# Optimization experiments

Measured on AMD Instinct MI355X. Metric: run time of the kernel, lower is better.

The kernel has to match this reference:

```python
import jax, jax.numpy as jnp
import numpy as np

N_VARS = 2048
N_LAYERS = 8
NODES = 4096
FAN_IN = 4
BATCH = 8192


def setup_inputs() -> dict:
    key = jax.random.key(0)
    k1, k2 = jax.random.split(key)
    x = jax.random.uniform(k1, (BATCH, N_VARS), dtype=jnp.float32)
    marginalized_variables = jnp.zeros((N_VARS,), dtype=bool)
    # child_idx[l, n, f]: index of the f-th child of node n in layer l,
    # pointing into the previous layer's 4096 outputs (leaves for l=0).
    child_idx = jax.random.randint(k2, (N_LAYERS, NODES, FAN_IN), 0, NODES, dtype=jnp.int64)
    return {"x": x, "marginalized_variables": marginalized_variables, "child_idx": child_idx}


def reference(x, marginalized_variables, child_idx):
    # Leaf literals: positive literal = x[:, v], negative literal = 1 - x[:, v].
    # Marginalized variables output 1.0 for both literals.
    leaves = jnp.concatenate([x, 1.0 - x], axis=1)            # [B, 2V]
    marg = jnp.tile(marginalized_variables, 2)                 # [2V]
    cur = jnp.where(marg[None, :], jnp.ones((), dtype=leaves.dtype), leaves)
    n_layers = child_idx.shape[0]
    for l in range(n_layers):  # fixed small layer loop; each layer fully vectorized
        gathered = cur[:, child_idx[l]]                        # [B, NODES, FAN_IN]
        if l % 2 == 0:  # AND layer: product of children
            cur = jnp.prod(gathered, axis=-1)                  # [B, NODES]
        else:            # OR layer: sum of children
            cur = jnp.sum(gathered, axis=-1)                   # [B, NODES]
    # Root OR node over the final layer -> [B, 1]
    return jnp.sum(cur, axis=1, keepdims=True)
```

## Files before the change

### kernel.cpp

```cpp
#include <hip/hip_runtime.h>

constexpr int N_VARS   = 2048;
constexpr int NODES    = 4096;
constexpr int N_LAYERS = 8;
constexpr int BATCH    = 8192;
constexpr int THREADS  = 256;
constexpr int RPB      = 2;
constexpr int NPT      = NODES / THREADS;

__device__ __forceinline__ float bflo(unsigned w) { return __uint_as_float(w << 16); }
__device__ __forceinline__ float bfhi(unsigned w) { return __uint_as_float(w & 0xffff0000u); }
__device__ __forceinline__ unsigned bfpack(float a, float b) {
  unsigned ua = __float_as_uint(a), ub = __float_as_uint(b);
  ua = (ua + 0x7fffu + ((ua >> 16) & 1u)) >> 16;
  ub = (ub + 0x7fffu + ((ub >> 16) & 1u)) & 0xffff0000u;
  return ua | ub;
}

template <int MODE>
__device__ __forceinline__ ushort4 get_idx(const void* p, int n) {
  if (MODE == 0) return ((const ushort4*)p)[n];
  if (MODE == 1) {
    int4 c = ((const int4*)p)[n];
    return make_ushort4((unsigned short)c.x, (unsigned short)c.y,
                        (unsigned short)c.z, (unsigned short)c.w);
  }
  const int* q = (const int*)p + (size_t)n * 8;
  return make_ushort4((unsigned short)q[0], (unsigned short)q[2],
                      (unsigned short)q[4], (unsigned short)q[6]);
}
template <int MODE> __device__ __forceinline__ size_t layer_bytes() {
  return MODE == 0 ? (size_t)NODES * 8 : MODE == 1 ? (size_t)NODES * 16
                                                   : (size_t)NODES * 32;
}

template <int MODE>
__device__ __forceinline__ void prod_pass(const float2* A, unsigned* B,
                                          const void* idx, int t) {
#pragma unroll
  for (int i = 0; i < NPT; ++i) {
    const int n = t + i * THREADS;
    ushort4 c = get_idx<MODE>(idx, n);
    float2 a = A[c.x], b = A[c.y], d = A[c.z], e = A[c.w];
    B[n] = bfpack(a.x * b.x * d.x * e.x, a.y * b.y * d.y * e.y);
  }
}

template <int MODE>
__device__ __forceinline__ void sum_pass(const unsigned* B, float2* A,
                                         const void* idx, int t) {
#pragma unroll
  for (int i = 0; i < NPT; ++i) {
    const int n = t + i * THREADS;
    ushort4 c = get_idx<MODE>(idx, n);
    unsigned a = B[c.x], b = B[c.y], d = B[c.z], e = B[c.w];
    A[n] = make_float2(bflo(a) + bflo(b) + bflo(d) + bflo(e),
                       bfhi(a) + bfhi(b) + bfhi(d) + bfhi(e));
  }
}

template <int MODE>
__device__ __forceinline__ void spn_body(const float* __restrict__ x,
                                         const unsigned char* __restrict__ marg,
                                         const void* __restrict__ idx,
                                         float* __restrict__ out,
                                         float2* A,
                                         unsigned* B) {
  const int t = threadIdx.x;
  const int row0 = blockIdx.x * RPB;
  const float* x0 = x + (size_t)row0 * N_VARS;
  const float* x1 = x0 + N_VARS;

#pragma unroll
  for (int i = 0; i < N_VARS / THREADS; ++i) {
    const int j = t + i * THREADS;
    const float a = x0[j], b = x1[j];
    const bool m = marg[j] != 0;
    A[j]          = make_float2(m ? 1.f : a,       m ? 1.f : b);
    A[N_VARS + j] = make_float2(m ? 1.f : 1.f - a, m ? 1.f : 1.f - b);
  }

  const char* ib = (const char*)idx;
  const size_t LB = layer_bytes<MODE>();
  __syncthreads();
  prod_pass<MODE>(A, B, ib + 0 * LB, t); __syncthreads();
  sum_pass <MODE>(B, A, ib + 1 * LB, t); __syncthreads();
  prod_pass<MODE>(A, B, ib + 2 * LB, t); __syncthreads();
  sum_pass <MODE>(B, A, ib + 3 * LB, t); __syncthreads();
  prod_pass<MODE>(A, B, ib + 4 * LB, t); __syncthreads();
  sum_pass <MODE>(B, A, ib + 5 * LB, t); __syncthreads();
  prod_pass<MODE>(A, B, ib + 6 * LB, t); __syncthreads();

  float s0 = 0.f, s1 = 0.f;
  {
    const void* L7 = ib + 7 * LB;
#pragma unroll
    for (int i = 0; i < NPT; ++i) {
      const int n = t + i * THREADS;
      ushort4 c = get_idx<MODE>(L7, n);
      unsigned a = B[c.x], b = B[c.y], d = B[c.z], e = B[c.w];
      s0 += bflo(a) + bflo(b) + bflo(d) + bflo(e);
      s1 += bfhi(a) + bfhi(b) + bfhi(d) + bfhi(e);
    }
  }
#pragma unroll
  for (int off = 32; off > 0; off >>= 1) {
    s0 += __shfl_down(s0, off);
    s1 += __shfl_down(s1, off);
  }
  if ((t & 63) == 0) A[t >> 6] = make_float2(s0, s1);
  __syncthreads();
  if (t == 0) {
    float2 tot = A[0];
#pragma unroll
    for (int w = 1; w < THREADS / 64; ++w) { tot.x += A[w].x; tot.y += A[w].y; }
    out[row0]     = tot.x;
    out[row0 + 1] = tot.y;
  }
}

__global__ __launch_bounds__(THREADS) void spn_packed(
    const float* __restrict__ x, const unsigned char* __restrict__ marg,
    const ushort4* __restrict__ idx, float* __restrict__ out) {
  __shared__ float2   A[NODES];
  __shared__ unsigned B[NODES];
  spn_body<0>(x, marg, idx, out, A, B);
}

__global__ __launch_bounds__(THREADS) void spn_raw(
    const float* __restrict__ x, const unsigned char* __restrict__ marg,
    const int* __restrict__ cidx, float* __restrict__ out) {
  __shared__ float2   A[NODES];
  __shared__ unsigned B[NODES];
  int acc = 0;
#pragma unroll
  for (int k = 0; k < 8; ++k) acc |= cidx[2 * k + 1];
  if (acc == 0) spn_body<2>(x, marg, cidx, out, A, B);
  else          spn_body<1>(x, marg, cidx, out, A, B);
}

__global__ void pack_idx(const int* __restrict__ cidx, ushort4* __restrict__ out) {
  const int g = blockIdx.x * blockDim.x + threadIdx.x;
  int acc = 0;
#pragma unroll
  for (int k = 0; k < 8; ++k) acc |= cidx[2 * k + 1];
  ushort4 r;
  if (acc == 0) {
    const int* p = cidx + (size_t)g * 8;
    r = make_ushort4((unsigned short)p[0], (unsigned short)p[2],
                     (unsigned short)p[4], (unsigned short)p[6]);
  } else {
    int4 c = ((const int4*)cidx)[g];
    r = make_ushort4((unsigned short)c.x, (unsigned short)c.y,
                     (unsigned short)c.z, (unsigned short)c.w);
  }
  out[g] = r;
}

extern "C" void kernel_launch(void* const* d_in, const int* in_sizes, int n_in,
                              void* d_out, int out_size, void* d_ws, size_t ws_size,
                              hipStream_t stream) {
  const float* x          = (const float*)d_in[0];
  const unsigned char* mg = (const unsigned char*)d_in[1];
  const int* cidx         = (const int*)d_in[2];
  float* out              = (float*)d_out;

  const size_t need = (size_t)N_LAYERS * NODES * sizeof(ushort4);
  if (ws_size >= need) {
    ushort4* packed = (ushort4*)d_ws;
    hipLaunchKernelGGL(pack_idx, dim3((N_LAYERS * NODES) / 256), dim3(256), 0, stream,
                       cidx, packed);
    hipLaunchKernelGGL(spn_packed, dim3(BATCH / RPB), dim3(THREADS), 0, stream,
                       x, mg, packed, out);
  } else {
    hipLaunchKernelGGL(spn_raw, dim3(BATCH / RPB), dim3(THREADS), 0, stream,
                       x, mg, cidx, out);
  }
}
```

Before: 202.0 us.

## Reorder child indices to cut LDS bank conflicts, prescale offsets, use hw bf16 pack

```diff
diff --git a/kernel.cpp b/kernel.cpp
--- a/kernel.cpp
+++ b/kernel.cpp
@@ -4,30 +4,30 @@
 constexpr int NODES    = 4096;
 constexpr int N_LAYERS = 8;
 constexpr int BATCH    = 8192;
-constexpr int THREADS  = 256;
+constexpr int THREADS  = 512;
 constexpr int RPB      = 2;
 constexpr int NPT      = NODES / THREADS;
 
 __device__ __forceinline__ float bflo(unsigned w) { return __uint_as_float(w << 16); }
 __device__ __forceinline__ float bfhi(unsigned w) { return __uint_as_float(w & 0xffff0000u); }
-__device__ __forceinline__ unsigned bfpack(float a, float b) {
-  unsigned ua = __float_as_uint(a), ub = __float_as_uint(b);
-  ua = (ua + 0x7fffu + ((ua >> 16) & 1u)) >> 16;
-  ub = (ub + 0x7fffu + ((ub >> 16) & 1u)) & 0xffff0000u;
-  return ua | ub;
-}
-
-template <int MODE>
-__device__ __forceinline__ ushort4 get_idx(const void* p, int n) {
+
+__device__ __forceinline__ unsigned bfpack(float lo, float hi) {
+  unsigned r;
+  asm("v_cvt_pk_bf16_f32 %0, %1, %2" : "=v"(r) : "v"(lo), "v"(hi));
+  return r;
+}
+
+template <int MODE, int SHIFT>
+__device__ __forceinline__ ushort4 get_off(const void* p, int n) {
   if (MODE == 0) return ((const ushort4*)p)[n];
   if (MODE == 1) {
     int4 c = ((const int4*)p)[n];
-    return make_ushort4((unsigned short)c.x, (unsigned short)c.y,
-                        (unsigned short)c.z, (unsigned short)c.w);
+    return make_ushort4((unsigned short)(c.x << SHIFT), (unsigned short)(c.y << SHIFT),
+                        (unsigned short)(c.z << SHIFT), (unsigned short)(c.w << SHIFT));
   }
   const int* q = (const int*)p + (size_t)n * 8;
-  return make_ushort4((unsigned short)q[0], (unsigned short)q[2],
-                      (unsigned short)q[4], (unsigned short)q[6]);
+  return make_ushort4((unsigned short)(q[0] << SHIFT), (unsigned short)(q[2] << SHIFT),
+                      (unsigned short)(q[4] << SHIFT), (unsigned short)(q[6] << SHIFT));
 }
 template <int MODE> __device__ __forceinline__ size_t layer_bytes() {
   return MODE == 0 ? (size_t)NODES * 8 : MODE == 1 ? (size_t)NODES * 16
@@ -37,11 +37,15 @@
 template <int MODE>
 __device__ __forceinline__ void prod_pass(const float2* A, unsigned* B,
                                           const void* idx, int t) {
+  const char* Ab = (const char*)A;
 #pragma unroll
   for (int i = 0; i < NPT; ++i) {
     const int n = t + i * THREADS;
-    ushort4 c = get_idx<MODE>(idx, n);
-    float2 a = A[c.x], b = A[c.y], d = A[c.z], e = A[c.w];
+    ushort4 c = get_off<MODE, 3>(idx, n);
+    float2 a = *(const float2*)(Ab + c.x);
+    float2 b = *(const float2*)(Ab + c.y);
+    float2 d = *(const float2*)(Ab + c.z);
+    float2 e = *(const float2*)(Ab + c.w);
     B[n] = bfpack(a.x * b.x * d.x * e.x, a.y * b.y * d.y * e.y);
   }
 }
@@ -49,11 +53,15 @@
 template <int MODE>
 __device__ __forceinline__ void sum_pass(const unsigned* B, float2* A,
                                          const void* idx, int t) {
+  const char* Bb = (const char*)B;
 #pragma unroll
   for (int i = 0; i < NPT; ++i) {
     const int n = t + i * THREADS;
-    ushort4 c = get_idx<MODE>(idx, n);
-    unsigned a = B[c.x], b = B[c.y], d = B[c.z], e = B[c.w];
+    ushort4 c = get_off<MODE, 2>(idx, n);
+    unsigned a = *(const unsigned*)(Bb + c.x);
+    unsigned b = *(const unsigned*)(Bb + c.y);
+    unsigned d = *(const unsigned*)(Bb + c.z);
+    unsigned e = *(const unsigned*)(Bb + c.w);
     A[n] = make_float2(bflo(a) + bflo(b) + bflo(d) + bflo(e),
                        bfhi(a) + bfhi(b) + bfhi(d) + bfhi(e));
   }
@@ -94,11 +102,15 @@
   float s0 = 0.f, s1 = 0.f;
   {
     const void* L7 = ib + 7 * LB;
+    const char* Bb = (const char*)B;
 #pragma unroll
     for (int i = 0; i < NPT; ++i) {
       const int n = t + i * THREADS;
-      ushort4 c = get_idx<MODE>(L7, n);
-      unsigned a = B[c.x], b = B[c.y], d = B[c.z], e = B[c.w];
+      ushort4 c = get_off<MODE, 2>(L7, n);
+      unsigned a = *(const unsigned*)(Bb + c.x);
+      unsigned b = *(const unsigned*)(Bb + c.y);
+      unsigned d = *(const unsigned*)(Bb + c.z);
+      unsigned e = *(const unsigned*)(Bb + c.w);
       s0 += bflo(a) + bflo(b) + bflo(d) + bflo(e);
       s1 += bfhi(a) + bfhi(b) + bfhi(d) + bfhi(e);
     }
@@ -139,22 +151,72 @@
   else          spn_body<1>(x, marg, cidx, out, A, B);
 }
 
-__global__ void pack_idx(const int* __restrict__ cidx, ushort4* __restrict__ out) {
-  const int g = blockIdx.x * blockDim.x + threadIdx.x;
+__global__ __launch_bounds__(64) void pack_idx(const int* __restrict__ cidx,
+                                               ushort4* __restrict__ out) {
+  __shared__ unsigned short cnt[64][4][32];
+  const int tid   = threadIdx.x;
+  const int gid   = blockIdx.x * 64 + tid;
+  const int layer = gid >> 6;
+  const int group = gid & 63;
+  const int shift = (layer & 1) ? 2 : 3;
+  const int mask  = (layer & 1) ? 31 : 15;
+
   int acc = 0;
 #pragma unroll
   for (int k = 0; k < 8; ++k) acc |= cidx[2 * k + 1];
-  ushort4 r;
-  if (acc == 0) {
-    const int* p = cidx + (size_t)g * 8;
-    r = make_ushort4((unsigned short)p[0], (unsigned short)p[2],
-                     (unsigned short)p[4], (unsigned short)p[6]);
-  } else {
-    int4 c = ((const int4*)cidx)[g];
-    r = make_ushort4((unsigned short)c.x, (unsigned short)c.y,
-                     (unsigned short)c.z, (unsigned short)c.w);
-  }
-  out[g] = r;
+  const bool is64 = (acc == 0);
+
+#pragma unroll
+  for (int s = 0; s < 4; ++s)
+#pragma unroll
+    for (int b = 0; b < 32; ++b) cnt[tid][s][b] = 0;
+
+  constexpr unsigned char P24[24][4] = {
+      {0,1,2,3},{0,1,3,2},{0,2,1,3},{0,2,3,1},{0,3,1,2},{0,3,2,1},
+      {1,0,2,3},{1,0,3,2},{1,2,0,3},{1,2,3,0},{1,3,0,2},{1,3,2,0},
+      {2,0,1,3},{2,0,3,1},{2,1,0,3},{2,1,3,0},{2,3,0,1},{2,3,1,0},
+      {3,0,1,2},{3,0,2,1},{3,1,0,2},{3,1,2,0},{3,2,0,1},{3,2,1,0}};
+
+  const int n0 = group * 64;
+  for (int k = 0; k < 64; ++k) {
+    const int node = n0 + k;
+    int cv[4];
+    if (is64) {
+      const int* q = cidx + (size_t)(layer * NODES + node) * 8;
+      cv[0] = q[0]; cv[1] = q[2]; cv[2] = q[4]; cv[3] = q[6];
+    } else {
+      int4 v = ((const int4*)cidx)[layer * NODES + node];
+      cv[0] = v.x; cv[1] = v.y; cv[2] = v.z; cv[3] = v.w;
+    }
+    int bn[4];
+#pragma unroll
+    for (int j = 0; j < 4; ++j) bn[j] = cv[j] & mask;
+    int m2[4][4];
+#pragma unroll
+    for (int s = 0; s < 4; ++s)
+#pragma unroll
+      for (int j = 0; j < 4; ++j) {
+        const int v = cnt[tid][s][bn[j]];
+        m2[s][j] = v * v;
+      }
+    int bestc = 0x7fffffff;
+    int o0 = cv[0], o1 = cv[1], o2 = cv[2], o3 = cv[3];
+    int b0 = bn[0], b1 = bn[1], b2 = bn[2], b3 = bn[3];
+#pragma unroll
+    for (int p = 0; p < 24; ++p) {
+      const int j0 = P24[p][0], j1 = P24[p][1], j2 = P24[p][2], j3 = P24[p][3];
+      const int cost = m2[0][j0] + m2[1][j1] + m2[2][j2] + m2[3][j3];
+      if (cost < bestc) {
+        bestc = cost;
+        o0 = cv[j0]; o1 = cv[j1]; o2 = cv[j2]; o3 = cv[j3];
+        b0 = bn[j0]; b1 = bn[j1]; b2 = bn[j2]; b3 = bn[j3];
+      }
+    }
+    cnt[tid][0][b0]++; cnt[tid][1][b1]++; cnt[tid][2][b2]++; cnt[tid][3][b3]++;
+    out[layer * NODES + node] =
+        make_ushort4((unsigned short)(o0 << shift), (unsigned short)(o1 << shift),
+                     (unsigned short)(o2 << shift), (unsigned short)(o3 << shift));
+  }
 }
 
 extern "C" void kernel_launch(void* const* d_in, const int* in_sizes, int n_in,
@@ -168,8 +230,7 @@
   const size_t need = (size_t)N_LAYERS * NODES * sizeof(ushort4);
   if (ws_size >= need) {
     ushort4* packed = (ushort4*)d_ws;
-    hipLaunchKernelGGL(pack_idx, dim3((N_LAYERS * NODES) / 256), dim3(256), 0, stream,
-                       cidx, packed);
+    hipLaunchKernelGGL(pack_idx, dim3(8), dim3(64), 0, stream, cidx, packed);
     hipLaunchKernelGGL(spn_packed, dim3(BATCH / RPB), dim3(THREADS), 0, stream,
                        x, mg, packed, out);
   } else {
```

New measurement: 256.3 us. 26.9% more time.
